# Optimization experiments

Hardware: AMD Instinct MI355X
Metric: run time of the kernel (lower is better)

Reference implementation:

```python
import jax, jax.numpy as jnp
import numpy as np
from jax import lax

DIM = 384
NUM_HEADS = 8
KV_NUM_HEADS = 2
REP = NUM_HEADS // KV_NUM_HEADS  # 4
KV_DIM = DIM * 2 // REP          # 192
EPS_LN = 1e-5
EPS_NORM = 1e-12


def _layernorm_channel(x, w, b):
    # WithBias LayerNorm over channel dim of NCHW tensor (matches to_3d -> LN(c) -> to_4d)
    mu = jnp.mean(x, axis=1, keepdims=True)
    var = jnp.var(x, axis=1, keepdims=True)
    return (x - mu) / jnp.sqrt(var + EPS_LN) * w[None, :, None, None] + b[None, :, None, None]


def _conv1x1(x, w):
    # w: [out, in] ; x: [b, in, h, w]
    return jnp.einsum('oi,bihw->bohw', w, x)


def _dwconv3x3(x, w):
    # depthwise 3x3, padding=1; w: [C, 1, 3, 3]
    C = x.shape[1]
    return lax.conv_general_dilated(
        x, w, window_strides=(1, 1), padding=((1, 1), (1, 1)),
        feature_group_count=C,
        dimension_numbers=('NCHW', 'OIHW', 'NCHW'))


def _l2norm(x):
    n = jnp.linalg.norm(x, axis=-1, keepdims=True)
    return x / jnp.maximum(n, EPS_NORM)


def setup_inputs() -> dict:
    key = jax.random.key(0)
    ks = jax.random.split(key, 8)
    b, h, w = 8, 128, 128
    scale1 = 1.0 / np.sqrt(DIM)
    return {
        'q': jax.random.normal(ks[0], (b, DIM, h, w), dtype=jnp.float32),
        'k': jax.random.normal(ks[1], (b, DIM, h, w), dtype=jnp.float32),
        'w_q': jax.random.normal(ks[2], (DIM, DIM), dtype=jnp.float32) * scale1,
        'w_kv': jax.random.normal(ks[3], (KV_DIM, DIM), dtype=jnp.float32) * scale1,
        'w_q_dw': jax.random.normal(ks[4], (DIM, 1, 3, 3), dtype=jnp.float32) * (1.0 / 3.0),
        'w_kv_dw': jax.random.normal(ks[5], (KV_DIM, 1, 3, 3), dtype=jnp.float32) * (1.0 / 3.0),
        'w_out': jax.random.normal(ks[6], (DIM, DIM), dtype=jnp.float32) * scale1,
        'temperature': jnp.ones((NUM_HEADS, 1, 1), dtype=jnp.float32),
        'lnq_w': jnp.ones((DIM,), dtype=jnp.float32),
        'lnq_b': jnp.zeros((DIM,), dtype=jnp.float32),
        'lnk_w': jnp.ones((DIM,), dtype=jnp.float32),
        'lnk_b': jnp.zeros((DIM,), dtype=jnp.float32),
    }


def reference(q, k, w_q, w_kv, w_q_dw, w_kv_dw, w_out, temperature,
              lnq_w, lnq_b, lnk_w, lnk_b):
    b, c, h, w = q.shape
    hw = h * w
    qn = _layernorm_channel(q, lnq_w, lnq_b)
    kn = _layernorm_channel(k, lnk_w, lnk_b)
    qp = _dwconv3x3(_conv1x1(qn, w_q), w_q_dw)          # [b, dim, h, w]
    kv = _dwconv3x3(_conv1x1(kn, w_kv), w_kv_dw)        # [b, 2*dim/rep, h, w]
    kk, vv = jnp.split(kv, 2, axis=1)                   # each [b, dim/rep, h, w]
    # reshape to heads: channel-attention layout [b, head, c_head, hw]
    qh = qp.reshape(b, NUM_HEADS, DIM // NUM_HEADS, hw)
    kh = kk.reshape(b, KV_NUM_HEADS, DIM // NUM_HEADS, hw)
    vh = vv.reshape(b, KV_NUM_HEADS, DIM // NUM_HEADS, hw)
    # GQA repeat kv heads (repeat_interleave on head dim)
    kh = jnp.repeat(kh, REP, axis=1)
    vh = jnp.repeat(vh, REP, axis=1)
    qh = _l2norm(qh)
    kh = _l2norm(kh)
    attn = jnp.einsum('bhck,bhdk->bhcd', qh, kh) * temperature[None]
    attn = jax.nn.softmax(attn, axis=-1)
    out = jnp.einsum('bhcd,bhdk->bhck', attn, vh)       # [b, head, c_head, hw]
    out = out.reshape(b, DIM, h, w)
    return _conv1x1(out, w_out)
```

## Files before the change

kernel.cpp:

```cpp
#include <hip/hip_runtime.h>
#include <math.h>


typedef unsigned short u16;
typedef unsigned int u32;
typedef short s16x8 __attribute__((ext_vector_type(8)));
typedef float f32x4 __attribute__((ext_vector_type(4)));

#define HW 16384
#define NB 8
#define CDIM 384
#define KVC 192

__device__ __forceinline__ float b2f(u16 u) {
  return __uint_as_float(((u32)u) << 16);
}
__device__ __forceinline__ u16 f2b(float f) {
  u32 u = __float_as_uint(f);
  u += 0x7fffu + ((u >> 16) & 1u);
  return (u16)(u >> 16);
}
__device__ __forceinline__ u32 pack2(float a, float c) {
  return (u32)f2b(a) | ((u32)f2b(c) << 16);
}

__global__ void k0_prep(const float* __restrict__ wq, const float* __restrict__ wkv,
                        const float* __restrict__ wo,
                        const float* __restrict__ lnqw, const float* __restrict__ lnqb,
                        const float* __restrict__ lnkw, const float* __restrict__ lnkb,
                        u16* __restrict__ wqp, float* __restrict__ rwsQ, float* __restrict__ biasQ,
                        u16* __restrict__ wkvp, float* __restrict__ rwsKV, float* __restrict__ biasKV,
                        u16* __restrict__ wop) {
  int r = blockIdx.x * 256 + threadIdx.x;
  if (r < 384) {
    float rs = 0.f, bs = 0.f;
    for (int i = 0; i < 384; ++i) {
      float wp = wq[r * 384 + i] * lnqw[i];
      u16 h = f2b(wp);
      rs += b2f(h);
      bs += wq[r * 384 + i] * lnqb[i];
      wqp[r * 384 + i] = h;
    }
    rwsQ[r] = rs; biasQ[r] = bs;
  } else if (r < 640) {
    int o = r - 384;
    if (o < 192) {
      float rs = 0.f, bs = 0.f;
      for (int i = 0; i < 384; ++i) {
        float wp = wkv[o * 384 + i] * lnkw[i];
        u16 h = f2b(wp);
        rs += b2f(h);
        bs += wkv[o * 384 + i] * lnkb[i];
        wkvp[o * 384 + i] = h;
      }
      rwsKV[o] = rs; biasKV[o] = bs;
    } else {
      for (int i = 0; i < 384; ++i) wkvp[o * 384 + i] = 0;
      rwsKV[o] = 0.f; biasKV[o] = 0.f;
    }
  } else {
    int o = r - 640;
    for (int i = 0; i < 384; ++i) wop[o * 384 + i] = f2b(wo[o * 384 + i]);
  }
}

template <int MODE, int WM, int WN, int MF, int NF>
__global__ __launch_bounds__(512) void gemm_fused(const u16* __restrict__ A,
                                                  const void* __restrict__ Bsrc,
                                                  const float* __restrict__ rowsum,
                                                  const float* __restrict__ bias,
                                                  void* __restrict__ outv, int M) {
  __shared__ u16 tB[64 * 384];
  __shared__ float sredS[8][64], sredQ[8][64];
  __shared__ float muL[64], sdL[64];

  const int b = blockIdx.z, pt = blockIdx.x;
  const int tid = threadIdx.x;
  const int w = tid >> 6, l = tid & 63;
  const int wm = (WN == 1) ? w : (w >> 1);
  const int wn = (WN == 1) ? 0 : (w & 1);
  const int lr = l & 15, lg = l >> 4;

  f32x4 acc[MF][NF] = {};

  if (MODE == 0) {
    const float* Bf = (const float*)Bsrc;
    const size_t fbase = (size_t)b * CDIM * HW + (size_t)pt * 64 + l;
    float s_ = 0.f, q_ = 0.f;
#pragma unroll
    for (int it = 0; it < 12; ++it) {
      float v[4];
#pragma unroll
      for (int j = 0; j < 4; ++j)
        v[j] = Bf[fbase + (size_t)(it * 32 + w * 4 + j) * HW];
#pragma unroll
      for (int j = 0; j < 4; ++j) { s_ += v[j]; q_ += v[j] * v[j]; }
      u32 lo = pack2(v[0], v[1]), hi = pack2(v[2], v[3]);
      int cidx = it * 4 + (w >> 1);
      int off = l * 384 + ((cidx ^ (l & 7)) << 3) + (w & 1) * 4;
      *(uint2*)&tB[off] = make_uint2(lo, hi);
    }
    sredS[w][l] = s_;
    sredQ[w][l] = q_;
  } else {
    const u16* Bh = (const u16*)Bsrc;
#pragma unroll
    for (int i = 0; i < 6; ++i) {
      int chunk = tid + i * 512;
      int row = chunk / 48, c = chunk % 48;
      uint4 v = *(const uint4*)(Bh + ((size_t)(b * HW + pt * 64 + row)) * 384 + c * 8);
      *(uint4*)&tB[row * 384 + ((c ^ (row & 7)) << 3)] = v;
    }
  }
  __syncthreads();

  if (MODE == 0) {
    if (tid < 64) {
      float s = 0.f, q2 = 0.f;
#pragma unroll
      for (int g = 0; g < 8; ++g) { s += sredS[g][tid]; q2 += sredQ[g][tid]; }
      float mn = s * (1.f / 384.f);
      float var = q2 * (1.f / 384.f) - mn * mn;
      muL[tid] = mn;
      sdL[tid] = rsqrtf(var + 1e-5f);
    }
    __syncthreads();
  }

#pragma unroll
  for (int ks = 0; ks < 12; ++ks) {
    const int ko = ks * 32 + lg * 8;
    const int cidx = ks * 4 + lg;
    s16x8 a[MF], bb[NF];
#pragma unroll
    for (int mf = 0; mf < MF; ++mf)
      a[mf] = *(const s16x8*)(A + (size_t)(wm * (MF * 16) + mf * 16 + lr) * 384 + ko);
#pragma unroll
    for (int nf = 0; nf < NF; ++nf) {
      int row = wn * (NF * 16) + nf * 16 + lr;
      bb[nf] = *(const s16x8*)&tB[row * 384 + ((cidx ^ (row & 7)) << 3)];
    }
#pragma unroll
    for (int mf = 0; mf < MF; ++mf)
#pragma unroll
      for (int nf = 0; nf < NF; ++nf)
        acc[mf][nf] = __builtin_amdgcn_mfma_f32_16x16x32_bf16(a[mf], bb[nf], acc[mf][nf], 0, 0, 0);
  }

#pragma unroll
  for (int nf = 0; nf < NF; ++nf) {
    int row = wn * (NF * 16) + nf * 16 + lr;
    int p = pt * 64 + row;
    float m_ = 0.f, s_ = 0.f;
    if (MODE == 0) { m_ = muL[row]; s_ = sdL[row]; }
#pragma unroll
    for (int mf = 0; mf < MF; ++mf) {
#pragma unroll
      for (int r = 0; r < 4; ++r) {
        int o = wm * (MF * 16) + mf * 16 + lg * 4 + r;
        if (MODE == 0) {
          float v = s_ * (acc[mf][nf][r] - m_ * rowsum[o]) + bias[o];
          ((u16*)outv)[((size_t)(b * M + o)) * HW + p] = f2b(v);
        } else {
          ((float*)outv)[((size_t)(b * CDIM + o)) * HW + p] = acc[mf][nf][r];
        }
      }
    }
  }
}

__global__ __launch_bounds__(256) void k4_dw(const u16* __restrict__ qp, const u16* __restrict__ kvp,
                                             const float* __restrict__ wqdw, const float* __restrict__ wkvdw,
                                             u16* __restrict__ qd, u16* __restrict__ kvd,
                                             float* __restrict__ rnq, float* __restrict__ rnk) {
  __shared__ u16 plane[16384];
  __shared__ float red[256];

  int c = blockIdx.x, b = blockIdx.y;
  int tid = threadIdx.x;
  const u16* in; u16* outb; const float* wp; int C;
  int isQ = (c < 384), cc = isQ ? c : c - 384;
  if (isQ) { in = qp; outb = qd; wp = wqdw + cc * 9; C = CDIM; }
  else     { in = kvp; outb = kvd; wp = wkvdw + cc * 9; C = KVC; }
  size_t base = ((size_t)(b * C + cc)) * HW;

  float w[9];
#pragma unroll
  for (int j = 0; j < 9; ++j) w[j] = wp[j];

  const uint4* gsrc = (const uint4*)(in + base);
  uint4* lplane = (uint4*)plane;
#pragma unroll
  for (int i = 0; i < 8; ++i) lplane[tid + i * 256] = gsrc[tid + i * 256];
  __syncthreads();

  uint4* gdst = (uint4*)(outb + base);
  float ns = 0.f;
#pragma unroll
  for (int it = 0; it < 8; ++it) {
    int idx = tid + it * 256;
    int y = idx >> 4, ox = idx & 15;
    int x0 = ox * 8;

    float r[3][10];
#pragma unroll
    for (int rr = 0; rr < 3; ++rr) {
      int yy = y + rr - 1;
      if ((unsigned)yy < 128u) {
        int rbase = yy * 128 + x0;
        r[rr][0] = (x0 > 0) ? b2f(plane[rbase - 1]) : 0.f;
        uint4 v = *(const uint4*)&plane[rbase];
        u32 ws[4] = {v.x, v.y, v.z, v.w};
#pragma unroll
        for (int j = 0; j < 4; ++j) {
          r[rr][1 + 2 * j] = b2f((u16)(ws[j] & 0xffff));
          r[rr][2 + 2 * j] = b2f((u16)(ws[j] >> 16));
        }
        r[rr][9] = (x0 < 120) ? b2f(plane[rbase + 8]) : 0.f;
      } else {
#pragma unroll
        for (int j = 0; j < 10; ++j) r[rr][j] = 0.f;
      }
    }

    u32 packed[4];
#pragma unroll
    for (int j = 0; j < 8; ++j) {
      float a = 0.f;
#pragma unroll
      for (int rr = 0; rr < 3; ++rr)
#pragma unroll
        for (int dx = 0; dx < 3; ++dx)
          a += w[rr * 3 + dx] * r[rr][j + dx];
      u16 h = f2b(a);
      float hv = b2f(h);
      ns += hv * hv;
      if (j & 1) packed[j >> 1] |= ((u32)h) << 16; else packed[j >> 1] = (u32)h;
    }
    gdst[idx] = make_uint4(packed[0], packed[1], packed[2], packed[3]);
  }

  red[tid] = ns;
  __syncthreads();
  for (int st = 128; st > 0; st >>= 1) {
    if (tid < st) red[tid] += red[tid + st];
    __syncthreads();
  }
  if (tid == 0) {
    float n = sqrtf(red[0]);
    float inv = 1.f / fmaxf(n, 1e-12f);
    if (isQ) rnq[b * 384 + cc] = inv;
    else if (cc < 96) rnk[b * 96 + cc] = inv;
  }
}

__global__ void k5b_vt(const u16* __restrict__ kvd, u16* __restrict__ vt) {
  int p = blockIdx.x * 256 + threadIdx.x;
  int b = blockIdx.y;
  size_t sb = ((size_t)(b * KVC + 96)) * HW + p;
  uint4* dv = (uint4*)vt + ((size_t)(b * HW + p)) * 12;
  for (int j8 = 0; j8 < 12; ++j8) {
    u32 w[4];
#pragma unroll
    for (int j = 0; j < 8; ++j) {
      u16 h = kvd[sb + (size_t)(j8 * 8 + j) * HW];
      if (j & 1) w[j >> 1] |= ((u32)h) << 16; else w[j >> 1] = (u32)h;
    }
    dv[j8] = make_uint4(w[0], w[1], w[2], w[3]);
  }
}

__global__ __launch_bounds__(256) void k6_qk(const u16* __restrict__ qd,
                                             const u16* __restrict__ kvd,
                                             float* __restrict__ spart) {
  int kc = blockIdx.x, h = blockIdx.y, b = blockIdx.z;
  int tid = threadIdx.x;
  int w = tid >> 6, l = tid & 63, lr = l & 15, lg = l >> 4;
  int g = h >> 2;
  int p0 = kc * 1024 + w * 256;

  f32x4 acc[3][3] = {};
  size_t qbase = ((size_t)(b * CDIM + h * 48 + lr)) * HW;
  size_t kbase = ((size_t)(b * KVC + g * 48 + lr)) * HW;

  for (int ks = 0; ks < 8; ++ks) {
    int pp = p0 + ks * 32 + lg * 8;
    s16x8 a[3], bb[3];
#pragma unroll
    for (int mi = 0; mi < 3; ++mi) a[mi] = *(const s16x8*)(qd + qbase + (size_t)mi * 16 * HW + pp);
#pragma unroll
    for (int ni = 0; ni < 3; ++ni) bb[ni] = *(const s16x8*)(kvd + kbase + (size_t)ni * 16 * HW + pp);
#pragma unroll
    for (int mi = 0; mi < 3; ++mi)
#pragma unroll
      for (int ni = 0; ni < 3; ++ni)
        acc[mi][ni] = __builtin_amdgcn_mfma_f32_16x16x32_bf16(a[mi], bb[ni], acc[mi][ni], 0, 0, 0);
  }

  size_t sb = ((size_t)((((b * 8 + h) * 16) + kc) * 4 + w)) * 2304;
#pragma unroll
  for (int mi = 0; mi < 3; ++mi)
#pragma unroll
    for (int ni = 0; ni < 3; ++ni)
#pragma unroll
      for (int r = 0; r < 4; ++r) {
        int c = mi * 16 + lg * 4 + r, d = ni * 16 + lr;
        spart[sb + c * 48 + d] = acc[mi][ni][r];
      }
}

__global__ void k7_sm(const float* __restrict__ spart, const float* __restrict__ temp,
                      const float* __restrict__ rnq, const float* __restrict__ rnk,
                      u16* __restrict__ ptil) {
  int h = blockIdx.x, b = blockIdx.y, tid = threadIdx.x;
  int g = h >> 2;
  __shared__ float S[2304];
  size_t base = ((size_t)((b * 8 + h) * 64)) * 2304;
  for (int e = tid; e < 2304; e += 64) {
    float s = 0.f;
    for (int j = 0; j < 64; ++j) s += spart[base + (size_t)j * 2304 + e];
    S[e] = s;
  }
  __syncthreads();
  if (tid < 48) {
    int c = tid;
    float sq = temp[h] * rnq[b * 384 + h * 48 + c];
    float mx = -1e30f;
    for (int d = 0; d < 48; ++d) {
      float v = S[c * 48 + d] * sq * rnk[b * 96 + g * 48 + d];
      mx = fmaxf(mx, v);
    }
    float sum = 0.f;
    for (int d = 0; d < 48; ++d) {
      float v = S[c * 48 + d] * sq * rnk[b * 96 + g * 48 + d];
      sum += __expf(v - mx);
    }
    float inv = 1.f / sum;
    u16* row = ptil + ((size_t)(b * 384 + h * 48 + c)) * 96;
    for (int dk = 0; dk < 96; ++dk) {
      int d = dk - g * 48;
      float pv = 0.f;
      if (d >= 0 && d < 48) {
        float v = S[c * 48 + d] * sq * rnk[b * 96 + g * 48 + d];
        pv = __expf(v - mx) * inv;
      }
      row[dk] = f2b(pv);
    }
  }
}

__global__ __launch_bounds__(512) void k8_pv(const u16* __restrict__ vt,
                                             const u16* __restrict__ ptil,
                                             u16* __restrict__ yt) {
  int ptb = blockIdx.x, b = blockIdx.y;
  int tid = threadIdx.x;
  int w = tid >> 6, l = tid & 63, lr = l & 15, lg = l >> 4;
  int wm = w >> 2, wn = w & 3;

  f32x4 acc[4][6] = {};
  size_t arow0 = ((size_t)(b * HW + ptb * 128 + wm * 64 + lr)) * 96;
  size_t brow0 = ((size_t)(b * CDIM + wn * 96 + lr)) * 96;

  for (int ks = 0; ks < 3; ++ks) {
    int ko = ks * 32 + lg * 8;
    s16x8 a[4], bb[6];
#pragma unroll
    for (int mf = 0; mf < 4; ++mf) a[mf] = *(const s16x8*)(vt + arow0 + (size_t)mf * 16 * 96 + ko);
#pragma unroll
    for (int nf = 0; nf < 6; ++nf) bb[nf] = *(const s16x8*)(ptil + brow0 + (size_t)nf * 16 * 96 + ko);
#pragma unroll
    for (int mf = 0; mf < 4; ++mf)
#pragma unroll
      for (int nf = 0; nf < 6; ++nf)
        acc[mf][nf] = __builtin_amdgcn_mfma_f32_16x16x32_bf16(a[mf], bb[nf], acc[mf][nf], 0, 0, 0);
  }

#pragma unroll
  for (int mf = 0; mf < 4; ++mf)
#pragma unroll
    for (int nf = 0; nf < 6; ++nf)
#pragma unroll
      for (int r = 0; r < 4; ++r) {
        int p = ptb * 128 + wm * 64 + mf * 16 + lg * 4 + r;
        int c = wn * 96 + nf * 16 + lr;
        yt[((size_t)(b * HW + p)) * 384 + c] = f2b(acc[mf][nf][r]);
      }
}

extern "C" void kernel_launch(void* const* d_in, const int* in_sizes, int n_in,
                              void* d_out, int out_size, void* d_ws, size_t ws_size,
                              hipStream_t stream) {
  const float* q    = (const float*)d_in[0];
  const float* k    = (const float*)d_in[1];
  const float* w_q  = (const float*)d_in[2];
  const float* w_kv = (const float*)d_in[3];
  const float* w_qd = (const float*)d_in[4];
  const float* w_kd = (const float*)d_in[5];
  const float* w_o  = (const float*)d_in[6];
  const float* temp = (const float*)d_in[7];
  const float* lnqw = (const float*)d_in[8];
  const float* lnqb = (const float*)d_in[9];
  const float* lnkw = (const float*)d_in[10];
  const float* lnkb = (const float*)d_in[11];
  float* out = (float*)d_out;

  char* ws = (char*)d_ws;
  size_t off = 0;
  auto alloc = [&](size_t bytes) -> void* {
    void* p = ws + off;
    off += (bytes + 255) & ~(size_t)255;
    return p;
  };

  u16*   wqp   = (u16*)alloc(384 * 384 * 2);
  float* rwsQ  = (float*)alloc(384 * 4);
  float* biasQ = (float*)alloc(384 * 4);
  u16*   wkvp  = (u16*)alloc(256 * 384 * 2);
  float* rwsKV = (float*)alloc(256 * 4);
  float* biasKV= (float*)alloc(256 * 4);
  u16*   wop   = (u16*)alloc(384 * 384 * 2);
  u16*   qp    = (u16*)alloc((size_t)NB * CDIM * HW * 2);
  u16*   kvp   = (u16*)alloc((size_t)NB * KVC * HW * 2);
  u16*   qd    = (u16*)alloc((size_t)NB * CDIM * HW * 2);
  u16*   kvd   = (u16*)alloc((size_t)NB * KVC * HW * 2);
  u16*   vt    = (u16*)alloc((size_t)NB * HW * 96 * 2);
  float* spart = (float*)alloc((size_t)4096 * 2304 * 4);
  u16*   ptil  = (u16*)alloc((size_t)NB * CDIM * 96 * 2);
  float* rnq   = (float*)alloc((size_t)NB * 384 * 4);
  float* rnk   = (float*)alloc((size_t)NB * 96 * 4);

  u16* yt = qp;

  k0_prep<<<4, 256, 0, stream>>>(w_q, w_kv, w_o, lnqw, lnqb, lnkw, lnkb,
                                 wqp, rwsQ, biasQ, wkvp, rwsKV, biasKV, wop);

  gemm_fused<0, 8, 1, 3, 4><<<dim3(256, 1, NB), 512, 0, stream>>>(wqp, q, rwsQ, biasQ, qp, 384);
  gemm_fused<0, 4, 2, 3, 2><<<dim3(256, 1, NB), 512, 0, stream>>>(wkvp, k, rwsKV, biasKV, kvp, 192);

  k4_dw<<<dim3(576, NB), 256, 0, stream>>>(qp, kvp, w_qd, w_kd, qd, kvd, rnq, rnk);

  k5b_vt<<<dim3(64, NB), 256, 0, stream>>>(kvd, vt);

  k6_qk<<<dim3(16, 8, NB), 256, 0, stream>>>(qd, kvd, spart);
  k7_sm<<<dim3(8, NB), 64, 0, stream>>>(spart, temp, rnq, rnk, ptil);

  k8_pv<<<dim3(128, NB), 512, 0, stream>>>(vt, ptil, yt);

  gemm_fused<1, 8, 1, 3, 4><<<dim3(256, 1, NB), 512, 0, stream>>>(wop, yt, nullptr, nullptr, out, 384);
}
```

Baseline: 630.1 us.

## Stage GEMM epilogue through LDS for coalesced 16-byte stores and swizzle tile order

Previously the GEMM epilogue wrote each accumulator element directly to global memory as scattered 2-byte or 4-byte stores. It now writes results into a shared-memory staging buffer reused from the B tile, then copies out contiguous 16-byte vectors per output row. The fp32 output mode stages in two halves because of the LDS size limit. The block-to-pixel-tile mapping is also permuted so that consecutive blocks touch spread-out pixel tiles. This costs extra barriers and LDS traffic in exchange for much better store coalescing.

```diff
diff --git a/kernel.cpp b/kernel.cpp
--- a/kernel.cpp
+++ b/kernel.cpp
@@ -70,11 +70,18 @@
                                                   const float* __restrict__ rowsum,
                                                   const float* __restrict__ bias,
                                                   void* __restrict__ outv, int M) {
-  __shared__ u16 tB[64 * 384];
-  __shared__ float sredS[8][64], sredQ[8][64];
+  __shared__ __align__(16) char smem[57344];
+  u16*   tB    = (u16*)smem;
+  float* sredS = (float*)(smem + 49152);
+  float* sredQ = (float*)(smem + 53248);
+  u16*   chB16 = (u16*)smem;
+  float* chB32 = (float*)smem;
   __shared__ float muL[64], sdL[64];
 
-  const int b = blockIdx.z, pt = blockIdx.x;
+  constexpr int M_TILE = WM * MF * 16;
+
+  const int b = blockIdx.z;
+  const int pt = ((blockIdx.x & 7) << 5) | (blockIdx.x >> 3);
   const int tid = threadIdx.x;
   const int w = tid >> 6, l = tid & 63;
   const int wm = (WN == 1) ? w : (w >> 1);
@@ -100,8 +107,8 @@
       int off = l * 384 + ((cidx ^ (l & 7)) << 3) + (w & 1) * 4;
       *(uint2*)&tB[off] = make_uint2(lo, hi);
     }
-    sredS[w][l] = s_;
-    sredQ[w][l] = q_;
+    sredS[w * 64 + l] = s_;
+    sredQ[w * 64 + l] = q_;
   } else {
     const u16* Bh = (const u16*)Bsrc;
 #pragma unroll
@@ -118,7 +125,7 @@
     if (tid < 64) {
       float s = 0.f, q2 = 0.f;
 #pragma unroll
-      for (int g = 0; g < 8; ++g) { s += sredS[g][tid]; q2 += sredQ[g][tid]; }
+      for (int g = 0; g < 8; ++g) { s += sredS[g * 64 + tid]; q2 += sredQ[g * 64 + tid]; }
       float mn = s * (1.f / 384.f);
       float var = q2 * (1.f / 384.f) - mn * mn;
       muL[tid] = mn;
@@ -147,23 +154,50 @@
         acc[mf][nf] = __builtin_amdgcn_mfma_f32_16x16x32_bf16(a[mf], bb[nf], acc[mf][nf], 0, 0, 0);
   }
 
-#pragma unroll
-  for (int nf = 0; nf < NF; ++nf) {
-    int row = wn * (NF * 16) + nf * 16 + lr;
-    int p = pt * 64 + row;
-    float m_ = 0.f, s_ = 0.f;
-    if (MODE == 0) { m_ = muL[row]; s_ = sdL[row]; }
-#pragma unroll
-    for (int mf = 0; mf < MF; ++mf) {
-#pragma unroll
-      for (int r = 0; r < 4; ++r) {
-        int o = wm * (MF * 16) + mf * 16 + lg * 4 + r;
-        if (MODE == 0) {
-          float v = s_ * (acc[mf][nf][r] - m_ * rowsum[o]) + bias[o];
-          ((u16*)outv)[((size_t)(b * M + o)) * HW + p] = f2b(v);
-        } else {
-          ((float*)outv)[((size_t)(b * CDIM + o)) * HW + p] = acc[mf][nf][r];
+  if (MODE == 0) {
+    __syncthreads();
+#pragma unroll
+    for (int nf = 0; nf < NF; ++nf) {
+      int prow = wn * (NF * 16) + nf * 16 + lr;
+      float m_ = muL[prow], s_ = sdL[prow];
+#pragma unroll
+      for (int mf = 0; mf < MF; ++mf)
+#pragma unroll
+        for (int r = 0; r < 4; ++r) {
+          int orow = wm * (MF * 16) + mf * 16 + lg * 4 + r;
+          float v = s_ * (acc[mf][nf][r] - m_ * rowsum[orow]) + bias[orow];
+          chB16[orow * 72 + prow] = f2b(v);
         }
+    }
+    __syncthreads();
+    const int total = M_TILE * 8;
+    for (int i = tid; i < total; i += 512) {
+      int row = i >> 3, c8 = i & 7;
+      uint4 v = *(const uint4*)&chB16[row * 72 + c8 * 8];
+      *(uint4*)((u16*)outv + ((size_t)(b * M + row)) * HW + pt * 64 + c8 * 8) = v;
+    }
+  } else {
+#pragma unroll
+    for (int cc = 0; cc < 2; ++cc) {
+      __syncthreads();
+      if ((wm >> 2) == cc) {
+#pragma unroll
+        for (int nf = 0; nf < NF; ++nf) {
+          int prow = wn * (NF * 16) + nf * 16 + lr;
+#pragma unroll
+          for (int mf = 0; mf < MF; ++mf)
+#pragma unroll
+            for (int r = 0; r < 4; ++r) {
+              int orow_l = (wm & 3) * (MF * 16) + mf * 16 + lg * 4 + r;
+              chB32[orow_l * 72 + prow] = acc[mf][nf][r];
+            }
+        }
+      }
+      __syncthreads();
+      for (int i = tid; i < 192 * 16; i += 512) {
+        int row = i >> 4, c4 = i & 15;
+        uint4 v = *(const uint4*)&chB32[row * 72 + c4 * 4];
+        *(uint4*)((float*)outv + ((size_t)(b * CDIM + cc * 192 + row)) * HW + pt * 64 + c4 * 4) = v;
       }
     }
   }
```

Measured after the change: 628.2 us. Within noise of the previous version (-0.3%).
